# Kernel optimization log

Hardware: AMD Instinct MI355X
Metric: run time of the kernel (lower is better)

The kernel has to match this reference:

```python
import jax, jax.numpy as jnp
import numpy as np

D_MODEL = 2048
N_HEADS = 16
HEAD_DIM = D_MODEL // N_HEADS
B, L = 2, 2048
ROPE_BASE = 10000.0
NEG_INF = -1e30


def _rope_cache(seq_len, head_dim):
    inv_freq = 1.0 / (ROPE_BASE ** (np.arange(0, head_dim, 2, dtype=np.float32) / head_dim))
    t = np.arange(seq_len, dtype=np.float32)
    freqs = np.outer(t, inv_freq)                      # (L, hd/2)
    emb = np.concatenate([freqs, freqs], axis=-1)      # (L, hd)
    return jnp.asarray(np.cos(emb)), jnp.asarray(np.sin(emb))


def setup_inputs() -> dict:
    key = jax.random.key(0)
    kx, kq, ko, kl = jax.random.split(key, 4)
    x = jax.random.normal(kx, (B, L, D_MODEL), dtype=jnp.float32)
    w_qkv = jax.random.normal(kq, (3 * D_MODEL, D_MODEL), dtype=jnp.float32) / np.sqrt(D_MODEL)
    w_out = jax.random.normal(ko, (D_MODEL, D_MODEL), dtype=jnp.float32) / np.sqrt(D_MODEL)
    # key-padding style keep-mask: keep first `lengths[b]` tokens (pos 0 always kept)
    lengths = jax.random.randint(kl, (B,), L // 2, L + 1)
    attn_keep_mask = jnp.arange(L)[None, :] < lengths[:, None]
    cos, sin = _rope_cache(L, HEAD_DIM)
    return {"x": x, "attn_keep_mask": attn_keep_mask, "cos": cos, "sin": sin,
            "w_qkv": w_qkv, "w_out": w_out}


def _rotate_half(t):
    h = t.shape[-1] // 2
    return jnp.concatenate([-t[..., h:], t[..., :h]], axis=-1)


def _apply_rope(t, cos, sin):
    # t: (B, H, L, hd); cos/sin: (L, hd)
    return t * cos[None, None] + _rotate_half(t) * sin[None, None]


def reference(x, attn_keep_mask, cos, sin, w_qkv, w_out):
    Bv, Lv, Dv = x.shape
    qkv = jnp.einsum('bld,ed->ble', x, w_qkv)                      # (B, L, 3D)
    q, k, v = jnp.split(qkv, 3, axis=-1)
    def heads(t):
        return t.reshape(Bv, Lv, N_HEADS, HEAD_DIM).transpose(0, 2, 1, 3)  # (B,H,L,hd)
    q, k, v = heads(q), heads(k), heads(v)
    q = _apply_rope(q, cos, sin)
    k = _apply_rope(k, cos, sin)
    scale = 1.0 / np.sqrt(HEAD_DIM)
    scores = jnp.einsum('bhqd,bhkd->bhqk', q, k) * scale            # (B,H,L,L)
    causal = jnp.tril(jnp.ones((Lv, Lv), dtype=bool))               # (L,L)
    allowed = causal[None, None] & attn_keep_mask[:, None, None, :]  # keep keys
    scores = jnp.where(allowed, scores, NEG_INF)
    probs = jax.nn.softmax(scores, axis=-1)
    attn = jnp.einsum('bhqk,bhkd->bhqd', probs, v)                  # (B,H,L,hd)
    out = attn.transpose(0, 2, 1, 3).reshape(Bv, Lv, Dv)
    out = jnp.where(attn_keep_mask[:, :, None], out, 0.0)
    return jnp.einsum('bld,ed->ble', out, w_out)
```

## Files before the change

### kernel.cpp

```cpp
#include <hip/hip_runtime.h>

typedef unsigned short u16;
typedef u16 u16x8 __attribute__((ext_vector_type(8)));
typedef u16 u16x4 __attribute__((ext_vector_type(4)));
typedef __bf16 bf16x8_t __attribute__((ext_vector_type(8)));
typedef float f32x4 __attribute__((ext_vector_type(4)));

#define GLOBAL_AS __attribute__((address_space(1)))
#define LDS_AS __attribute__((address_space(3)))

__device__ __forceinline__ float bf2f(u16 v) {
    return __uint_as_float(((unsigned int)v) << 16);
}
__device__ __forceinline__ u16 f2bf(float f) {
    unsigned int u = __float_as_uint(f);
    u += 0x7fff + ((u >> 16) & 1);
    return (u16)(u >> 16);
}

__device__ __forceinline__ f32x4 mfma_bf16(u16x8 a, u16x8 b, f32x4 c) {
    return __builtin_amdgcn_mfma_f32_16x16x32_bf16(
        __builtin_bit_cast(bf16x8_t, a), __builtin_bit_cast(bf16x8_t, b), c, 0, 0, 0);
}

__device__ __forceinline__ float red16_max(float x) {
    int t;
    t = __builtin_amdgcn_update_dpp(0, __builtin_bit_cast(int, x), 0xB1, 0xF, 0xF, true);
    x = fmaxf(x, __builtin_bit_cast(float, t));
    t = __builtin_amdgcn_update_dpp(0, __builtin_bit_cast(int, x), 0x4E, 0xF, 0xF, true);
    x = fmaxf(x, __builtin_bit_cast(float, t));
    t = __builtin_amdgcn_update_dpp(0, __builtin_bit_cast(int, x), 0x124, 0xF, 0xF, true);
    x = fmaxf(x, __builtin_bit_cast(float, t));
    t = __builtin_amdgcn_update_dpp(0, __builtin_bit_cast(int, x), 0x128, 0xF, 0xF, true);
    x = fmaxf(x, __builtin_bit_cast(float, t));
    return x;
}

__global__ __launch_bounds__(256) void cvt_kernel(const float* __restrict__ in,
                                                  u16* __restrict__ out, int n4) {
    int i = blockIdx.x * 256 + threadIdx.x;
    if (i >= n4) return;
    float4 f = ((const float4*)in)[i];
    u16x4 o = { f2bf(f.x), f2bf(f.y), f2bf(f.z), f2bf(f.w) };
    ((u16x4*)out)[i] = o;
}

__global__ __launch_bounds__(256) void mask_prep(const unsigned char* __restrict__ raw,
                                                 int* __restrict__ lens) {
    const int b = blockIdx.x;
    const int tid = threadIdx.x, lane = tid & 63, wid = tid >> 6;
    const unsigned char b0 = raw[0];
    int cnt = 0;
    for (int i = tid; i < 2048; i += 256) {
        const size_t idx = (size_t)b * 2048 + i;
        bool v;
        if (b0 == 0) {
            v = ((const float*)raw)[idx] != 0.0f;
        } else if (b0 == 0x80) {
            v = ((const u16*)raw)[idx] != 0;
        } else {
            const int stride = raw[1] ? 1 : (raw[2] ? 2 : (raw[4] ? 4 : 8));
            v = raw[idx * stride] != 0;
        }
        cnt += v ? 1 : 0;
    }
    cnt += __shfl_xor(cnt, 1);
    cnt += __shfl_xor(cnt, 2);
    cnt += __shfl_xor(cnt, 4);
    cnt += __shfl_xor(cnt, 8);
    cnt += __shfl_xor(cnt, 16);
    cnt += __shfl_xor(cnt, 32);
    __shared__ int wsum[4];
    if (lane == 0) wsum[wid] = cnt;
    __syncthreads();
    if (tid == 0) lens[b] = wsum[0] + wsum[1] + wsum[2] + wsum[3];
}

template <int MODE>
__global__ __launch_bounds__(512, 2) void gemm_bt(
    const u16* __restrict__ A, const u16* __restrict__ B,
    int M, int N, int K, int nbx,
    u16* __restrict__ qp, u16* __restrict__ kp, u16* __restrict__ vp,
    float* __restrict__ outf) {
    __shared__ u16 lds[3 * 24576];
    const int tid  = threadIdx.x;
    const int lane = tid & 63;
    const int wid  = tid >> 6;
    const int wm   = wid >> 1;
    const int wn   = wid & 1;

    const int bid = blockIdx.x;
    const int k8  = bid & 7;
    const int loc = bid >> 3;
    const int rbx = nbx >> 2;
    const int lbx = loc >> 3;
    const int lby = loc & 7;
    const int by  = (k8 >> 2) * 8 + lby;
    const int bx  = (k8 & 3) * rbx + lbx;
    const int brow = by * 256;
    const int bcol = bx * 128;

    f32x4 acc[4][4];
#pragma unroll
    for (int m = 0; m < 4; ++m)
#pragma unroll
        for (int n = 0; n < 4; ++n)
            acc[m][n] = (f32x4){0.f, 0.f, 0.f, 0.f};

    const int scol  = (((tid & 7) ^ ((tid >> 3) & 7)) << 3);
    const int arow0 = tid >> 3;
    const u16* aBase = A + (size_t)(brow + arow0) * K + scol;
    const u16* bBase = B + (size_t)(bcol + arow0) * K + scol;

    auto stage = [&](int kt, int bb) {
        char* base = (char*)lds + bb * 49152;
        const u16* as = aBase + kt * 64;
        const u16* bs = bBase + kt * 64;
#pragma unroll
        for (int i = 0; i < 4; ++i)
            __builtin_amdgcn_global_load_lds((const GLOBAL_AS void*)(as + (size_t)(i * 64) * K),
                (LDS_AS void*)(base + i * 8192 + wid * 1024), 16, 0, 0);
#pragma unroll
        for (int i = 0; i < 2; ++i)
            __builtin_amdgcn_global_load_lds((const GLOBAL_AS void*)(bs + (size_t)(i * 64) * K),
                (LDS_AS void*)(base + 32768 + i * 8192 + wid * 1024), 16, 0, 0);
    };

    const int nkt = K >> 6;
    stage(0, 0);
    stage(1, 1);

    int bufc = 0;
    for (int kt = 0; kt < nkt; ++kt) {
        if (kt + 1 < nkt) asm volatile("s_waitcnt vmcnt(6)" ::: "memory");
        else              asm volatile("s_waitcnt vmcnt(0)" ::: "memory");
        __builtin_amdgcn_s_barrier();
        __builtin_amdgcn_sched_barrier(0);

        if (kt + 2 < nkt) {
            int nb = bufc + 2; if (nb >= 3) nb -= 3;
            stage(kt + 2, nb);
        }

        const u16* lA = lds + bufc * 24576;
        const u16* lB = lA + 16384;
        u16x8 af[4][2], bfr[4][2];
#pragma unroll
        for (int m = 0; m < 4; ++m)
#pragma unroll
            for (int ks = 0; ks < 2; ++ks) {
                const int row = wm * 64 + m * 16 + (lane & 15);
                const int g = ((ks << 2) + (lane >> 4)) ^ (lane & 7);
                af[m][ks] = *(const u16x8*)&lA[row * 64 + (g << 3)];
            }
#pragma unroll
        for (int n = 0; n < 4; ++n)
#pragma unroll
            for (int ks = 0; ks < 2; ++ks) {
                const int row = wn * 64 + n * 16 + (lane & 15);
                const int g = ((ks << 2) + (lane >> 4)) ^ (lane & 7);
                bfr[n][ks] = *(const u16x8*)&lB[row * 64 + (g << 3)];
            }

        __builtin_amdgcn_s_setprio(1);
#pragma unroll
        for (int ks = 0; ks < 2; ++ks)
#pragma unroll
            for (int m = 0; m < 4; ++m)
#pragma unroll
                for (int n = 0; n < 4; ++n)
                    acc[m][n] = mfma_bf16(af[m][ks], bfr[n][ks], acc[m][n]);
        __builtin_amdgcn_s_setprio(0);

        ++bufc; if (bufc == 3) bufc = 0;
    }

#pragma unroll
    for (int m = 0; m < 4; ++m) {
#pragma unroll
        for (int n = 0; n < 4; ++n) {
#pragma unroll
            for (int j = 0; j < 4; ++j) {
                const int row = brow + wm * 64 + m * 16 + (lane >> 4) * 4 + j;
                const int col = bcol + wn * 64 + n * 16 + (lane & 15);
                const float val = acc[m][n][j];
                if (MODE == 0) {
                    const int part = col >> 11;
                    const int e = col & 2047;
                    const int hh = e >> 7, dd = e & 127;
                    const int bb = row >> 11, ll = row & 2047;
                    u16* dst = (part == 0) ? qp : (part == 1) ? kp : vp;
                    dst[((size_t)(bb * 16 + hh) * 2048 + ll) * 128 + dd] = f2bf(val);
                } else {
                    outf[(size_t)row * N + col] = val;
                }
            }
        }
    }
}

__global__ __launch_bounds__(256) void rope_kernel(u16* __restrict__ qk,
                                                   const float* __restrict__ cosp,
                                                   const float* __restrict__ sinp) {
    const int gid  = blockIdx.x * 4 + (threadIdx.x >> 6);
    const int lane = threadIdx.x & 63;
    const int l    = gid & 2047;
    u16* row = qk + (size_t)gid * 128;
    const int d1 = lane, d2 = lane + 64;
    const float v1 = bf2f(row[d1]);
    const float v2 = bf2f(row[d2]);
    const float c1 = cosp[l * 128 + d1], s1 = sinp[l * 128 + d1];
    const float c2 = cosp[l * 128 + d2], s2 = sinp[l * 128 + d2];
    row[d1] = f2bf(v1 * c1 - v2 * s1);
    row[d2] = f2bf(v2 * c2 + v1 * s2);
}

__global__ __launch_bounds__(256, 2) void attn_kernel(
    const u16* __restrict__ Q, const u16* __restrict__ K, const u16* __restrict__ V,
    const int* __restrict__ lens, u16* __restrict__ O) {
    __shared__ u16 lK[64 * 128];
    __shared__ u16 lVT[128 * 64];
    __shared__ u16 lP[4 * 16 * 64];

    const int tid = threadIdx.x, lane = tid & 63, wid = tid >> 6;
    const int g   = blockIdx.x;
    const int xcd = g & 7;
    const int r   = g >> 3;
    const int jq  = 31 - (r >> 2);
    const int bh  = (xcd << 2) | (r & 3);
    const int b   = bh >> 4;
    const int h   = bh & 15;
    const u16* qb = Q + (size_t)bh * 2048 * 128;
    const u16* kb = K + (size_t)bh * 2048 * 128;
    const u16* vb = V + (size_t)bh * 2048 * 128;
    const int lenb = lens[b];
    const int q0w = jq * 64 + wid * 16;
    const int str = lane;
    const int sdc = wid;
    const float scale2 = 0.12754245006257017f;
    const float THR = 32.0f;
    u16* lPw = lP + wid * 1024;

    if (jq * 64 >= lenb) {
#pragma unroll
        for (int j = 0; j < 4; ++j) {
            const int qq = q0w + (lane >> 4) * 4 + j;
#pragma unroll
            for (int n = 0; n < 8; ++n) {
                const int d = n * 16 + (lane & 15);
                O[((size_t)b * 2048 + qq) * 2048 + h * 128 + d] = 0;
            }
        }
        return;
    }

    const int nt_full = jq + 1;
    const int lt = (lenb + 63) >> 6;
    const int ktiles = nt_full < lt ? nt_full : lt;

    u16x8 aq[4];
#pragma unroll
    for (int kc = 0; kc < 4; ++kc)
        aq[kc] = *(const u16x8*)(qb + (size_t)(q0w + (lane & 15)) * 128 + kc * 32 + (lane >> 4) * 8);

    u16x8 ONES;
#pragma unroll
    for (int e = 0; e < 8; ++e) ONES[e] = 0x3F80;

    float ms[4];
    f32x4 ls4, alpha4;
    f32x4 ao[8];
#pragma unroll
    for (int j = 0; j < 4; ++j) ms[j] = 0.f;
    ls4 = (f32x4){0.f, 0.f, 0.f, 0.f};
#pragma unroll
    for (int n = 0; n < 8; ++n) ao[n] = (f32x4){0.f, 0.f, 0.f, 0.f};

    u16x8 pk[4], pv[4];
    {
        const u16* ks = kb + (size_t)str * 128 + sdc * 32;
        const u16* vs = vb + (size_t)str * 128 + sdc * 32;
#pragma unroll
        for (int i = 0; i < 4; ++i) { pk[i] = *(const u16x8*)(ks + i * 8); pv[i] = *(const u16x8*)(vs + i * 8); }
    }
#pragma unroll
    for (int i = 0; i < 4; ++i) {
        *(u16x8*)&lK[str * 128 + (((sdc * 4 + i) ^ (str & 7)) << 3)] = pk[i];
#pragma unroll
        for (int e = 0; e < 8; ++e) {
            const int d = sdc * 32 + i * 8 + e;
            lVT[d * 64 + (((str >> 3) ^ (d & 7)) << 3) + (str & 7)] = pv[i][e];
        }
    }
    __syncthreads();

    for (int t = 0; t < ktiles; ++t) {
        const bool pf = (t + 1 < ktiles);
        if (pf) {
            const u16* ks = kb + (size_t)((t + 1) * 64 + str) * 128 + sdc * 32;
            const u16* vs = vb + (size_t)((t + 1) * 64 + str) * 128 + sdc * 32;
#pragma unroll
            for (int i = 0; i < 4; ++i) { pk[i] = *(const u16x8*)(ks + i * 8); pv[i] = *(const u16x8*)(vs + i * 8); }
        }
        const int kv0 = t * 64;

        f32x4 sv4[4];
#pragma unroll
        for (int n = 0; n < 4; ++n) sv4[n] = (f32x4){0.f, 0.f, 0.f, 0.f};
#pragma unroll
        for (int kc = 0; kc < 4; ++kc) {
            u16x8 bk[4];
#pragma unroll
            for (int n = 0; n < 4; ++n) {
                const int rk = n * 16 + (lane & 15);
                bk[n] = *(const u16x8*)&lK[rk * 128 + (((kc * 4 + (lane >> 4)) ^ (rk & 7)) << 3)];
            }
#pragma unroll
            for (int n = 0; n < 4; ++n)
                sv4[n] = mfma_bf16(aq[kc], bk[n], sv4[n]);
        }

        const bool needmask = (t == jq) || (kv0 + 64 > lenb);
#pragma unroll
        for (int j = 0; j < 4; ++j) {
            const int row = (lane >> 4) * 4 + j;
            float sv[4];
            if (needmask) {
                const int qq = q0w + row;
                const int bound = (qq < lenb - 1) ? qq : (lenb - 1);
#pragma unroll
                for (int n = 0; n < 4; ++n) {
                    const int kk = kv0 + n * 16 + (lane & 15);
                    sv[n] = (kk <= bound) ? sv4[n][j] : -1e30f;
                }
            } else {
#pragma unroll
                for (int n = 0; n < 4; ++n) sv[n] = sv4[n][j];
            }
            const float mk = ms[j] * scale2;
#pragma unroll
            for (int n = 0; n < 4; ++n) {
                const float p = exp2f(fmaf(sv[n], scale2, -mk));
                lPw[row * 64 + (((n * 2 + ((lane & 15) >> 3)) ^ (row & 7)) << 3) + (lane & 7)] = f2bf(p);
            }
            const float rm = red16_max(fmaxf(fmaxf(sv[0], sv[1]), fmaxf(sv[2], sv[3])));
            const bool grow = !__all(rm <= ms[j] + THR);
            float a = 1.0f;
            if (grow) {
                const float mn = fmaxf(ms[j], rm);
                a = exp2f((ms[j] - mn) * scale2);
                ms[j] = mn;
            }
            alpha4[j] = a;
        }

#pragma unroll
        for (int kc = 0; kc < 2; ++kc) {
            const int rp = lane & 15;
            u16x8 ap = *(const u16x8*)&lPw[rp * 64 + (((kc * 4 + (lane >> 4)) ^ (rp & 7)) << 3)];
            ls4 = mfma_bf16(ap, ONES, ls4);
#pragma unroll
            for (int n = 0; n < 8; ++n) {
                const int rd = n * 16 + (lane & 15);
                u16x8 bv = *(const u16x8*)&lVT[rd * 64 + (((kc * 4 + (lane >> 4)) ^ (rd & 7)) << 3)];
                ao[n] = mfma_bf16(ap, bv, ao[n]);
            }
        }

        ls4 *= alpha4;
#pragma unroll
        for (int n = 0; n < 8; ++n) ao[n] *= alpha4;

        if (pf) {
            __syncthreads();
#pragma unroll
            for (int i = 0; i < 4; ++i) {
                *(u16x8*)&lK[str * 128 + (((sdc * 4 + i) ^ (str & 7)) << 3)] = pk[i];
#pragma unroll
                for (int e = 0; e < 8; ++e) {
                    const int d = sdc * 32 + i * 8 + e;
                    lVT[d * 64 + (((str >> 3) ^ (d & 7)) << 3) + (str & 7)] = pv[i][e];
                }
            }
            __syncthreads();
        }
    }

#pragma unroll
    for (int j = 0; j < 4; ++j) {
        const int qq = q0w + (lane >> 4) * 4 + j;
        const float inv = (qq < lenb) ? (1.f / ls4[j]) : 0.f;
#pragma unroll
        for (int n = 0; n < 8; ++n) {
            const int d = n * 16 + (lane & 15);
            O[((size_t)b * 2048 + qq) * 2048 + h * 128 + d] = f2bf(ao[n][j] * inv);
        }
    }
}

extern "C" void kernel_launch(void* const* d_in, const int* in_sizes, int n_in,
                              void* d_out, int out_size, void* d_ws, size_t ws_size,
                              hipStream_t stream) {
    const float* x      = (const float*)d_in[0];
    const unsigned char* maskraw = (const unsigned char*)d_in[1];
    const float* cosp   = (const float*)d_in[2];
    const float* sinp   = (const float*)d_in[3];
    const float* w_qkv  = (const float*)d_in[4];
    const float* w_out  = (const float*)d_in[5];
    float* out = (float*)d_out;

    char* ws = (char*)d_ws;
    size_t off = 0;
    auto alloc = [&](size_t bytes) {
        char* p = ws + off;
        off += (bytes + 255) & ~(size_t)255;
        return p;
    };
    u16* xb    = (u16*)alloc((size_t)4096 * 2048 * 2);
    u16* wqkvb = (u16*)alloc((size_t)6144 * 2048 * 2);
    u16* woutb = (u16*)alloc((size_t)2048 * 2048 * 2);
    u16* qB    = (u16*)alloc((size_t)65536 * 128 * 2);
    u16* kB    = (u16*)alloc((size_t)65536 * 128 * 2);
    u16* vB    = (u16*)alloc((size_t)65536 * 128 * 2);
    u16* attno = (u16*)alloc((size_t)4096 * 2048 * 2);
    int* lens  = (int*)alloc(256);

    cvt_kernel<<<dim3(4096 * 2048 / 4 / 256), dim3(256), 0, stream>>>(x, xb, 4096 * 2048 / 4);
    cvt_kernel<<<dim3(6144 * 2048 / 4 / 256), dim3(256), 0, stream>>>(w_qkv, wqkvb, 6144 * 2048 / 4);
    cvt_kernel<<<dim3(2048 * 2048 / 4 / 256), dim3(256), 0, stream>>>(w_out, woutb, 2048 * 2048 / 4);
    mask_prep<<<dim3(2), dim3(256), 0, stream>>>(maskraw, lens);

    gemm_bt<0><<<dim3(768), dim3(512), 0, stream>>>(xb, wqkvb, 4096, 6144, 2048, 48,
                                                    qB, kB, vB, nullptr);
    rope_kernel<<<dim3(131072 / 4), dim3(256), 0, stream>>>(qB, cosp, sinp);
    attn_kernel<<<dim3(1024), dim3(256), 0, stream>>>(qB, kB, vB, lens, attno);
    gemm_bt<1><<<dim3(256), dim3(512), 0, stream>>>(attno, woutb, 4096, 2048, 2048, 16,
                                                    nullptr, nullptr, nullptr, out);
}
```

Before: 261.1 us.

## Restructure GEMM to 128x256 tiles with double-buffered half-K staging

The bf16 GEMM block tile changes from 256x128 to 128x256, with a 2x4 wave grid in place of 4x2. The three-buffer 64-wide K pipeline becomes a two-buffer scheme that splits each K tile into two 32-wide halves. Each half is loaded, computed and prefetched on its own with a new pair-row swizzled LDS layout. This lowers LDS use and interleaves loads with MFMA at finer grain, but adds a second barrier per K tile and reduces prefetch depth.

```diff
diff --git a/kernel.cpp b/kernel.cpp
--- a/kernel.cpp
+++ b/kernel.cpp
@@ -79,26 +79,23 @@
 template <int MODE>
 __global__ __launch_bounds__(512, 2) void gemm_bt(
     const u16* __restrict__ A, const u16* __restrict__ B,
-    int M, int N, int K, int nbx,
+    int M, int N, int K, int rbx,
     u16* __restrict__ qp, u16* __restrict__ kp, u16* __restrict__ vp,
     float* __restrict__ outf) {
-    __shared__ u16 lds[3 * 24576];
+    __shared__ u16 lds[2 * 24576];
     const int tid  = threadIdx.x;
     const int lane = tid & 63;
     const int wid  = tid >> 6;
-    const int wm   = wid >> 1;
-    const int wn   = wid & 1;
+    const int wr   = wid >> 2;
+    const int wc   = wid & 3;
 
     const int bid = blockIdx.x;
     const int k8  = bid & 7;
     const int loc = bid >> 3;
-    const int rbx = nbx >> 2;
-    const int lbx = loc >> 3;
-    const int lby = loc & 7;
-    const int by  = (k8 >> 2) * 8 + lby;
-    const int bx  = (k8 & 3) * rbx + lbx;
-    const int brow = by * 256;
-    const int bcol = bx * 128;
+    const int by  = (k8 >> 2) * 16 + (loc & 15);
+    const int bx  = (k8 & 3) * rbx + (loc >> 4);
+    const int brow = by * 128;
+    const int bcol = bx * 256;
 
     f32x4 acc[4][4];
 #pragma unroll
@@ -107,72 +104,80 @@
         for (int n = 0; n < 4; ++n)
             acc[m][n] = (f32x4){0.f, 0.f, 0.f, 0.f};
 
-    const int scol  = (((tid & 7) ^ ((tid >> 3) & 7)) << 3);
-    const int arow0 = tid >> 3;
-    const u16* aBase = A + (size_t)(brow + arow0) * K + scol;
-    const u16* bBase = B + (size_t)(bcol + arow0) * K + scol;
-
-    auto stage = [&](int kt, int bb) {
-        char* base = (char*)lds + bb * 49152;
-        const u16* as = aBase + kt * 64;
-        const u16* bs = bBase + kt * 64;
-#pragma unroll
-        for (int i = 0; i < 4; ++i)
-            __builtin_amdgcn_global_load_lds((const GLOBAL_AS void*)(as + (size_t)(i * 64) * K),
-                (LDS_AS void*)(base + i * 8192 + wid * 1024), 16, 0, 0);
-#pragma unroll
-        for (int i = 0; i < 2; ++i)
-            __builtin_amdgcn_global_load_lds((const GLOBAL_AS void*)(bs + (size_t)(i * 64) * K),
-                (LDS_AS void*)(base + 32768 + i * 8192 + wid * 1024), 16, 0, 0);
+    const int s5   = (lane & 7) ^ (lane >> 3);
+    const int srow = (wid << 4) + 2 * (lane >> 3) + (s5 >> 2);
+    const int scol = (s5 & 3) << 3;
+    const u16* aS = A + (size_t)(brow + srow) * K + scol;
+    const u16* bS = B + (size_t)(bcol + srow) * K + scol;
+
+    auto stgA = [&](int kt, int kh, int bb) {
+        __builtin_amdgcn_global_load_lds(
+            (const GLOBAL_AS void*)(aS + (size_t)kt * 64 + kh * 32),
+            (LDS_AS void*)((char*)lds + bb * 49152 + kh * 8192 + wid * 1024), 16, 0, 0);
     };
+    auto stgB = [&](int kt, int kh, int bb) {
+        const u16* src = bS + (size_t)kt * 64 + kh * 32;
+        char* base = (char*)lds + bb * 49152 + 16384 + kh * 16384 + wid * 1024;
+        __builtin_amdgcn_global_load_lds((const GLOBAL_AS void*)src,
+            (LDS_AS void*)base, 16, 0, 0);
+        __builtin_amdgcn_global_load_lds((const GLOBAL_AS void*)(src + (size_t)128 * K),
+            (LDS_AS void*)(base + 8192), 16, 0, 0);
+    };
+
+    auto rdA = [&](int bb, int kh, int mi) -> u16x8 {
+        const int r  = wr * 64 + mi * 16 + (lane & 15);
+        const int pr = r >> 1;
+        const int g  = (((r & 1) << 2) + (lane >> 4)) ^ (pr & 7);
+        return *(const u16x8*)((const char*)lds + bb * 49152 + kh * 8192 + pr * 128 + g * 16);
+    };
+    auto rdB = [&](int bb, int kh, int ni) -> u16x8 {
+        const int r  = wc * 64 + ni * 16 + (lane & 15);
+        const int pr = r >> 1;
+        const int g  = (((r & 1) << 2) + (lane >> 4)) ^ (pr & 7);
+        return *(const u16x8*)((const char*)lds + bb * 49152 + 16384 + kh * 16384 + pr * 128 + g * 16);
+    };
 
     const int nkt = K >> 6;
-    stage(0, 0);
-    stage(1, 1);
-
-    int bufc = 0;
-    for (int kt = 0; kt < nkt; ++kt) {
-        if (kt + 1 < nkt) asm volatile("s_waitcnt vmcnt(6)" ::: "memory");
-        else              asm volatile("s_waitcnt vmcnt(0)" ::: "memory");
+    stgA(0, 0, 0); stgB(0, 0, 0);
+    stgA(0, 1, 0); stgB(0, 1, 0);
+
+    for (int t = 0; t < nkt; ++t) {
+        const int cur = t & 1;
+        const bool more = (t + 1 < nkt);
+        u16x8 af[4], bf[4];
+
+        asm volatile("s_waitcnt vmcnt(3)" ::: "memory");
         __builtin_amdgcn_s_barrier();
         __builtin_amdgcn_sched_barrier(0);
-
-        if (kt + 2 < nkt) {
-            int nb = bufc + 2; if (nb >= 3) nb -= 3;
-            stage(kt + 2, nb);
-        }
-
-        const u16* lA = lds + bufc * 24576;
-        const u16* lB = lA + 16384;
-        u16x8 af[4][2], bfr[4][2];
+#pragma unroll
+        for (int m = 0; m < 4; ++m) af[m] = rdA(cur, 0, m);
+#pragma unroll
+        for (int n = 0; n < 4; ++n) bf[n] = rdB(cur, 0, n);
+        if (more) { stgA(t + 1, 0, cur ^ 1); stgB(t + 1, 0, cur ^ 1); }
+        __builtin_amdgcn_s_setprio(1);
 #pragma unroll
         for (int m = 0; m < 4; ++m)
 #pragma unroll
-            for (int ks = 0; ks < 2; ++ks) {
-                const int row = wm * 64 + m * 16 + (lane & 15);
-                const int g = ((ks << 2) + (lane >> 4)) ^ (lane & 7);
-                af[m][ks] = *(const u16x8*)&lA[row * 64 + (g << 3)];
-            }
-#pragma unroll
-        for (int n = 0; n < 4; ++n)
-#pragma unroll
-            for (int ks = 0; ks < 2; ++ks) {
-                const int row = wn * 64 + n * 16 + (lane & 15);
-                const int g = ((ks << 2) + (lane >> 4)) ^ (lane & 7);
-                bfr[n][ks] = *(const u16x8*)&lB[row * 64 + (g << 3)];
-            }
-
+            for (int n = 0; n < 4; ++n)
+                acc[m][n] = mfma_bf16(af[m], bf[n], acc[m][n]);
+        __builtin_amdgcn_s_setprio(0);
+
+        if (more) asm volatile("s_waitcnt vmcnt(3)" ::: "memory");
+        else      asm volatile("s_waitcnt vmcnt(0)" ::: "memory");
+        __builtin_amdgcn_s_barrier();
+        __builtin_amdgcn_sched_barrier(0);
+#pragma unroll
+        for (int m = 0; m < 4; ++m) af[m] = rdA(cur, 1, m);
+#pragma unroll
+        for (int n = 0; n < 4; ++n) bf[n] = rdB(cur, 1, n);
+        if (more) { stgA(t + 1, 1, cur ^ 1); stgB(t + 1, 1, cur ^ 1); }
         __builtin_amdgcn_s_setprio(1);
 #pragma unroll
-        for (int ks = 0; ks < 2; ++ks)
-#pragma unroll
-            for (int m = 0; m < 4; ++m)
-#pragma unroll
-                for (int n = 0; n < 4; ++n)
-                    acc[m][n] = mfma_bf16(af[m][ks], bfr[n][ks], acc[m][n]);
+        for (int m = 0; m < 4; ++m)
+#pragma unroll
+            for (int n = 0; n < 4; ++n)
+                acc[m][n] = mfma_bf16(af[m], bf[n], acc[m][n]);
         __builtin_amdgcn_s_setprio(0);
-
-        ++bufc; if (bufc == 3) bufc = 0;
     }
 
 #pragma unroll
@@ -181,8 +186,8 @@
         for (int n = 0; n < 4; ++n) {
 #pragma unroll
             for (int j = 0; j < 4; ++j) {
-                const int row = brow + wm * 64 + m * 16 + (lane >> 4) * 4 + j;
-                const int col = bcol + wn * 64 + n * 16 + (lane & 15);
+                const int row = brow + wr * 64 + m * 16 + (lane >> 4) * 4 + j;
+                const int col = bcol + wc * 64 + n * 16 + (lane & 15);
                 const float val = acc[m][n][j];
                 if (MODE == 0) {
                     const int part = col >> 11;
@@ -430,10 +435,10 @@
     cvt_kernel<<<dim3(2048 * 2048 / 4 / 256), dim3(256), 0, stream>>>(w_out, woutb, 2048 * 2048 / 4);
     mask_prep<<<dim3(2), dim3(256), 0, stream>>>(maskraw, lens);
 
-    gemm_bt<0><<<dim3(768), dim3(512), 0, stream>>>(xb, wqkvb, 4096, 6144, 2048, 48,
+    gemm_bt<0><<<dim3(768), dim3(512), 0, stream>>>(xb, wqkvb, 4096, 6144, 2048, 6,
                                                     qB, kB, vB, nullptr);
     rope_kernel<<<dim3(131072 / 4), dim3(256), 0, stream>>>(qB, cosp, sinp);
     attn_kernel<<<dim3(1024), dim3(256), 0, stream>>>(qB, kB, vB, lens, attno);
-    gemm_bt<1><<<dim3(256), dim3(512), 0, stream>>>(attno, woutb, 4096, 2048, 2048, 16,
+    gemm_bt<1><<<dim3(256), dim3(512), 0, stream>>>(attno, woutb, 4096, 2048, 2048, 2,
                                                     nullptr, nullptr, nullptr, out);
 }
```

Result: no change. 264.3 us (+1.3%).
